# Performance work log

Measured on AMD Instinct MI355X. Metric: run time of the kernel, lower is better.

## Reference

```python
import jax, jax.numpy as jnp
import numpy as np
import math

# init kwargs (constants)
HSHIFT, VSHIFT, ANGLE = 2, 2, 2
BS, C, H, W = 2048, 1, 64, 64


def setup_inputs() -> dict:
    key = jax.random.key(0)
    k1, k2 = jax.random.split(key)
    fm1 = jax.random.normal(k1, (BS, C, H, W), dtype=jnp.float32)
    fm2 = jax.random.normal(k2, (BS, C, H, W), dtype=jnp.float32)
    return {"fm1": fm1, "fm2": fm2}


def _warp_rotate(img, theta_deg, h, w):
    """Equivalent of cv2.warpAffine(img, cv2.getRotationMatrix2D((w/2,h/2), theta, 1)).

    img: [bs, h, w]. Bilinear interpolation, constant-0 border.
    Returns (rotated_img [bs,h,w], rotated_ones_mask [h,w]).
    cv2 inverts the forward map internally; inverse of rotation by theta about
    the center is rotation by -theta about the center.
    """
    t = -theta_deg * (math.pi / 180.0)
    alpha = jnp.cos(t)
    beta = jnp.sin(t)
    cx, cy = w / 2.0, h / 2.0
    ys, xs = jnp.meshgrid(jnp.arange(h, dtype=jnp.float32),
                          jnp.arange(w, dtype=jnp.float32), indexing="ij")
    x_src = alpha * xs + beta * ys + (1.0 - alpha) * cx - beta * cy
    y_src = -beta * xs + alpha * ys + beta * cx + (1.0 - alpha) * cy

    x0 = jnp.floor(x_src)
    y0 = jnp.floor(y_src)
    wx = x_src - x0
    wy = y_src - y0
    x0i = x0.astype(jnp.int32)
    y0i = y0.astype(jnp.int32)

    out = jnp.zeros_like(img)
    msk = jnp.zeros((h, w), img.dtype)
    corners = ((0, 0, (1 - wy) * (1 - wx)), (0, 1, (1 - wy) * wx),
               (1, 0, wy * (1 - wx)), (1, 1, wy * wx))
    for dy, dx, wgt in corners:
        yi = y0i + dy
        xi = x0i + dx
        valid = ((yi >= 0) & (yi < h) & (xi >= 0) & (xi < w)).astype(img.dtype)
        yc = jnp.clip(yi, 0, h - 1)
        xc = jnp.clip(xi, 0, w - 1)
        out = out + (wgt * valid) * img[:, yc, xc]
        msk = msk + wgt * valid
    return out, msk


def _forward(fm1, fm2):
    bs, c, h, w = fm1.shape
    thetas = jnp.arange(-ANGLE, ANGLE + 1, dtype=jnp.float32)
    min_dist = jnp.full((bs,), jnp.finfo(jnp.float32).max, dtype=jnp.float32)
    for bh in range(-HSHIFT, HSHIFT + 1):
        for bv in range(-VSHIFT, VSHIFT + 1):
            if bh >= 0:
                r1, r2 = fm1[:, :, :, :w - bh], fm2[:, :, :, bh:]
            else:
                r1, r2 = fm1[:, :, :, -bh:], fm2[:, :, :, :w + bh]
            if bv >= 0:
                r1, r2 = r1[:, :, :h - bv, :], r2[:, :, bv:, :]
            else:
                r1, r2 = r1[:, :, -bv:, :], r2[:, :, :h + bv, :]
            oh, ow = r1.shape[2], r1.shape[3]
            r1s = r1[:, 0]  # [bs, oh, ow] (C==1)
            # original detaches ref2 before warping (cv2 path)
            r2s = jax.lax.stop_gradient(r2[:, 0])

            def one_theta(theta, r1s=r1s, r2s=r2s, oh=oh, ow=ow):
                rr2, mk = _warp_rotate(r2s, theta, oh, ow)
                se = ((r1s - rr2) ** 2) * mk  # [bs, oh, ow]
                return se.reshape(se.shape[0], -1).sum(1) / mk.sum()

            dists = jax.vmap(one_theta)(thetas)  # [ntheta, bs]
            min_dist = jnp.minimum(min_dist, dists.min(0))
    return min_dist


def reference(fm1, fm2):
    return _forward(fm1, fm2)
```

## Files before the change

kernel.cpp:

```cpp
#include <hip/hip_runtime.h>
#include <hip/hip_fp16.h>
#include <math.h>

#define NTH 5
#define GLO 66
#define GHI 132
#define PS (GLO + 4096 + GHI)

#define ALP0 0.99939082701909576f
#define ALP1 0.99984769515639127f
constexpr float ALPc[5] = {ALP0, ALP1, 1.0f, ALP1, ALP0};
constexpr float BETc[5] = {0.03489949670250097f, 0.01745240643728351f, 0.0f,
                           -0.01745240643728351f, -0.03489949670250097f};

__device__ __forceinline__ unsigned h2bits(float a, float b) {
    __half2 h = __floats2half2_rn(a, b);
    return *(unsigned*)&h;
}
__device__ __forceinline__ __half2 h2(unsigned u) { return *(__half2*)&u; }

__device__ __forceinline__ int pkadd(int a, int b) {
    __half2 r = __hadd2(*(__half2*)&a, *(__half2*)&b);
    return *(int*)&r;
}
__device__ __forceinline__ int hred16(__half2 v) {
    int x = *(int*)&v;
    int t = __builtin_amdgcn_update_dpp(0, x, 0xB1, 0xF, 0xF, true);
    x = pkadd(x, t);
    t = __builtin_amdgcn_update_dpp(0, x, 0x4E, 0xF, 0xF, true);
    x = pkadd(x, t);
    t = __builtin_amdgcn_update_dpp(0, x, 0x141, 0xF, 0xF, true);
    x = pkadd(x, t);
    t = __builtin_amdgcn_update_dpp(0, x, 0x140, 0xF, 0xF, true);
    x = pkadd(x, t);
    return x;
}

__global__ void pack_kernel(const float* __restrict__ fm1,
                            const float* __restrict__ fm2,
                            __half* __restrict__ fm1h,
                            __half* __restrict__ fm2h) {
    const int g = blockIdx.x;
    const int tid = threadIdx.x;
    const size_t inb = (size_t)g * 16 * 4096;
    for (int p = tid; p < 4096; p += 1024) {
        uint4 wa, wb, va, vb;
        wa.x = h2bits(fm1[inb + 0 * 4096 + p], fm1[inb + 1 * 4096 + p]);
        wa.y = h2bits(fm1[inb + 2 * 4096 + p], fm1[inb + 3 * 4096 + p]);
        wa.z = h2bits(fm1[inb + 4 * 4096 + p], fm1[inb + 5 * 4096 + p]);
        wa.w = h2bits(fm1[inb + 6 * 4096 + p], fm1[inb + 7 * 4096 + p]);
        wb.x = h2bits(fm1[inb + 8 * 4096 + p], fm1[inb + 9 * 4096 + p]);
        wb.y = h2bits(fm1[inb + 10 * 4096 + p], fm1[inb + 11 * 4096 + p]);
        wb.z = h2bits(fm1[inb + 12 * 4096 + p], fm1[inb + 13 * 4096 + p]);
        wb.w = h2bits(fm1[inb + 14 * 4096 + p], fm1[inb + 15 * 4096 + p]);
        va.x = h2bits(fm2[inb + 0 * 4096 + p], fm2[inb + 1 * 4096 + p]);
        va.y = h2bits(fm2[inb + 2 * 4096 + p], fm2[inb + 3 * 4096 + p]);
        va.z = h2bits(fm2[inb + 4 * 4096 + p], fm2[inb + 5 * 4096 + p]);
        va.w = h2bits(fm2[inb + 6 * 4096 + p], fm2[inb + 7 * 4096 + p]);
        vb.x = h2bits(fm2[inb + 8 * 4096 + p], fm2[inb + 9 * 4096 + p]);
        vb.y = h2bits(fm2[inb + 10 * 4096 + p], fm2[inb + 11 * 4096 + p]);
        vb.z = h2bits(fm2[inb + 12 * 4096 + p], fm2[inb + 13 * 4096 + p]);
        vb.w = h2bits(fm2[inb + 14 * 4096 + p], fm2[inb + 15 * 4096 + p]);
        *(uint4*)(fm1h + ((size_t)(g * 2 + 0) * 4096 + p) * 8) = wa;
        *(uint4*)(fm1h + ((size_t)(g * 2 + 1) * 4096 + p) * 8) = wb;
        *(uint4*)(fm2h + ((size_t)(g * 2 + 0) * 4096 + p) * 8) = va;
        *(uint4*)(fm2h + ((size_t)(g * 2 + 1) * 4096 + p) * 8) = vb;
    }
}

__global__ void table_kernel(uint4* __restrict__ tab, float* __restrict__ denom) {
    const int bid = blockIdx.x;
    const int s = bid >> 2, tj = bid & 3;
    const int ti = tj < 2 ? tj : tj + 1;
    const int tid = threadIdx.x;
    const int bh = (s / 5) - 2;
    const int bv = (s % 5) - 2;
    const int ox2 = bh >= 0 ? bh : 0;
    const int ow = 64 - (bh >= 0 ? bh : -bh);
    const int oy2 = bv >= 0 ? bv : 0;
    const int oh = 64 - (bv >= 0 ? bv : -bv);
    const float cx = 0.5f * (float)ow;
    const float cy = 0.5f * (float)oh;
    const float alpha = ALPc[ti], beta = BETc[ti];
    __shared__ float mred[4];
    float macc = 0.0f;
    for (int i = 0; i < 16; i++) {
        const int px = tid + 256 * i;
        const int y = px >> 6, x = px & 63;
        uint4 e = make_uint4(0u, 0u, 0u, (unsigned)GLO);
        if (x < ow && y < oh) {
            const float xs = (float)x, yf = (float)y;
            const float hx = fmaf(alpha, xs, (1.0f - alpha) * cx - beta * cy);
            const float hy = fmaf(-beta, xs, beta * cx + (1.0f - alpha) * cy);
            const float xsrc = fmaf(beta, yf, hx);
            const float ysrc = fmaf(alpha, yf, hy);
            const float x0f = floorf(xsrc), y0f = floorf(ysrc);
            const float wx = xsrc - x0f, wy = ysrc - y0f;
            const int x0 = (int)x0f, y0 = (int)y0f;
            const float ax0 = ((unsigned)x0 < (unsigned)ow) ? (1.f - wx) : 0.f;
            const float ax1 = ((unsigned)(x0 + 1) < (unsigned)ow) ? wx : 0.f;
            const float ay0 = ((unsigned)y0 < (unsigned)oh) ? (1.f - wy) : 0.f;
            const float ay1 = ((unsigned)(y0 + 1) < (unsigned)oh) ? wy : 0.f;
            const int x0c = min(max(x0, -1), ow - 1);
            const int y0c = min(max(y0, -1), oh - 1);
            const float mk = (ax0 + ax1) * (ay0 + ay1);
            e.x = h2bits(ay0 * ax0, ay0 * ax1);
            e.y = h2bits(ay1 * ax0, ay1 * ax1);
            e.z = h2bits(mk, 0.0f);
            e.w = (unsigned)(GLO + (y0c + oy2) * 64 + (x0c + ox2));
            macc += mk;
        }
        tab[(size_t)bid * 4096 + px] = e;
    }
    #pragma unroll
    for (int off = 32; off; off >>= 1) macc += __shfl_xor(macc, off);
    if ((tid & 63) == 0) mred[tid >> 6] = macc;
    __syncthreads();
    if (tid == 0) {
        denom[s * 5 + ti] = mred[0] + mred[1] + mred[2] + mred[3];
        if (tj == 0) denom[s * 5 + 2] = (float)(ow * oh);
    }
}

__launch_bounds__(1024, 8)
__global__ void wrsl_main(const __half* __restrict__ fm1h,
                          const __half* __restrict__ fm2h,
                          const uint4* __restrict__ tab,
                          const float* __restrict__ denom,
                          float* __restrict__ out) {
    __shared__ uint4 lds[PS];
    __shared__ float redm[16][4][40];
    __shared__ float colsum[40];

    const int tid = threadIdx.x;
    const int g = blockIdx.x >> 2;
    const int pl = (blockIdx.x >> 1) & 1;
    const int hf = blockIdx.x & 1;
    const int sBeg = hf ? 13 : 0;
    const int sEnd = hf ? 25 : 13;
    const size_t pbase = (size_t)(g * 2 + pl) * 4096;

    {
        const uint4* src = (const uint4*)(fm2h + pbase * 8);
        #pragma unroll
        for (int i = 0; i < 4; i++)
            lds[GLO + tid + 1024 * i] = src[tid + 1024 * i];
        if (tid < GLO + GHI) {
            const int off = (tid < GLO) ? tid : (4096 + tid);
            lds[off] = make_uint4(0u, 0u, 0u, 0u);
        }
    }
    const int lane = tid & 63, wid = tid >> 6;
    __syncthreads();

    float best = 3.4028234663852886e38f;

    for (int s = sBeg; s < sEnd; s++) {
        const int bh = (s / 5) - 2;
        const int bv = (s % 5) - 2;
        const int ox1 = bh >= 0 ? 0 : -bh;
        const int ox2 = bh >= 0 ? bh : 0;
        const int ow = 64 - (bh >= 0 ? bh : -bh);
        const int oy1 = bv >= 0 ? 0 : -bv;
        const int oy2 = bv >= 0 ? bv : 0;
        const int oh = 64 - (bv >= 0 ? bv : -bv);
        const int xcap = ox1 + min(lane, ow - 1);

        uint4 nr[4];
        #pragma unroll
        for (int k = 0; k < 4; k++) {
            const int p1 = (oy1 + min(wid + 16 * k, oh - 1)) * 64 + xcap;
            uint4 a = *(const uint4*)(fm1h + (pbase + p1) * 8);
            a.x ^= 0x80008000u; a.y ^= 0x80008000u; a.z ^= 0x80008000u; a.w ^= 0x80008000u;
            nr[k] = a;
        }

        const uint4* tqbase = tab + (size_t)(s * 4) * 4096;
        uint4 tv[4];
        #pragma unroll
        for (int k = 0; k < 4; k++)
            tv[k] = tqbase[(wid + 16 * k) * 64 + lane];

        {
            const float xinf = (lane < ow) ? 1.0f : 0.0f;
            const __half2 z2 = __float2half2_rn(0.0f);
            __half2 se[4] = {z2, z2, z2, z2};
            #pragma unroll
            for (int k = 0; k < 4; k++) {
                const int y = wid + 16 * k;
                const __half2 msk = __float2half2_rn((y < oh) ? xinf : 0.0f);
                const int idx = GLO + (oy2 + y) * 64 + ox2 + lane;
                const uint4 qa = lds[idx];
                #define LIGHT(SE, C)                                          \
                {                                                             \
                    __half2 d = __hmul2(__hadd2(h2(qa.C), h2(nr[k].C)), msk); \
                    SE = __hfma2(d, d, SE);                                   \
                }
                LIGHT(se[0], x) LIGHT(se[1], y) LIGHT(se[2], z) LIGHT(se[3], w)
                #undef LIGHT
            }
            int r0 = hred16(se[0]), r1 = hred16(se[1]);
            int r2 = hred16(se[2]), r3 = hred16(se[3]);
            if ((lane & 15) == 0) {
                float2 f0 = __half22float2(h2(r0)), f1 = __half22float2(h2(r1));
                float2 f2 = __half22float2(h2(r2)), f3 = __half22float2(h2(r3));
                float4* dst = (float4*)&redm[wid][lane >> 4][2 * 8];
                dst[0] = make_float4(f0.x, f0.y, f1.x, f1.y);
                dst[1] = make_float4(f2.x, f2.y, f3.x, f3.y);
            }
        }

        #pragma unroll
        for (int tj = 0; tj < 4; tj++) {
            const int ti = tj < 2 ? tj : tj + 1;
            uint4 tvn[4];
            if (tj < 3) {
                const uint4* tqn = tqbase + (size_t)(tj + 1) * 4096;
                #pragma unroll
                for (int k = 0; k < 4; k++)
                    tvn[k] = tqn[(wid + 16 * k) * 64 + lane];
            }

            const __half2 z2 = __float2half2_rn(0.0f);
            __half2 se[4] = {z2, z2, z2, z2};
            #pragma unroll
            for (int k = 0; k < 4; k++) {
                const __half2 tx = h2(tv[k].x), ty = h2(tv[k].y);
                const __half2 w00p = __low2half2(tx), w01p = __high2half2(tx);
                const __half2 w10p = __low2half2(ty), w11p = __high2half2(ty);
                const __half2 mkp = __low2half2(h2(tv[k].z));
                const int b0 = (int)tv[k].w;
                const uint4 q00 = lds[b0], q01 = lds[b0 + 1];
                const uint4 q10 = lds[b0 + 64], q11 = lds[b0 + 65];
                #define FULL(SE, C)                                        \
                {                                                          \
                    __half2 r = __hfma2(w00p, h2(q00.C), h2(nr[k].C));     \
                    r = __hfma2(w01p, h2(q01.C), r);                       \
                    r = __hfma2(w10p, h2(q10.C), r);                       \
                    r = __hfma2(w11p, h2(q11.C), r);                       \
                    SE = __hfma2(__hmul2(r, mkp), r, SE);                  \
                }
                FULL(se[0], x) FULL(se[1], y) FULL(se[2], z) FULL(se[3], w)
                #undef FULL
            }
            int r0 = hred16(se[0]), r1 = hred16(se[1]);
            int r2 = hred16(se[2]), r3 = hred16(se[3]);
            if ((lane & 15) == 0) {
                float2 f0 = __half22float2(h2(r0)), f1 = __half22float2(h2(r1));
                float2 f2 = __half22float2(h2(r2)), f3 = __half22float2(h2(r3));
                float4* dst = (float4*)&redm[wid][lane >> 4][ti * 8];
                dst[0] = make_float4(f0.x, f0.y, f1.x, f1.y);
                dst[1] = make_float4(f2.x, f2.y, f3.x, f3.y);
            }
            if (tj < 3) {
                #pragma unroll
                for (int k = 0; k < 4; k++) tv[k] = tvn[k];
            }
        }

        __syncthreads();
        if (tid < 40) {
            float sum = 0.0f;
            #pragma unroll 8
            for (int w = 0; w < 16; w++) {
                sum += redm[w][0][tid] + redm[w][1][tid] + redm[w][2][tid] + redm[w][3][tid];
            }
            colsum[tid] = sum;
        }
        __syncthreads();
        if (tid < 8) {
            #pragma unroll
            for (int t2 = 0; t2 < NTH; t2++)
                best = fminf(best, colsum[t2 * 8 + tid] / denom[s * 5 + t2]);
        }
    }
    if (tid < 8)
        atomicMin((unsigned int*)&out[g * 16 + pl * 8 + tid], __float_as_uint(best));
}

extern "C" void kernel_launch(void* const* d_in, const int* in_sizes, int n_in,
                              void* d_out, int out_size, void* d_ws, size_t ws_size,
                              hipStream_t stream) {
    const float* fm1 = (const float*)d_in[0];
    const float* fm2 = (const float*)d_in[1];
    float* out = (float*)d_out;
    __half* fm1h = (__half*)d_ws;
    __half* fm2h = (__half*)((char*)d_ws + (16u << 20));
    uint4* tab = (uint4*)((char*)d_ws + (32u << 20));
    float* denom = (float*)((char*)d_ws + (32u << 20) + 100u * 4096u * 16u);

    hipMemsetAsync(d_out, 0x7F, (size_t)out_size * 4, stream);
    pack_kernel<<<128, 1024, 0, stream>>>(fm1, fm2, fm1h, fm2h);
    table_kernel<<<100, 256, 0, stream>>>(tab, denom);
    wrsl_main<<<512, 1024, 0, stream>>>(fm1h, fm2h, tab, denom, out);
}
```

Measured before the change: 191.0 us.

## Split warp table into pre-broadcast weights and mask/index arrays, widen prep grids

Splits the per-pixel bilinear table into a 16-byte array of pre-broadcast half2 weights and an 8-byte mask/index array. This removes the per-use low/high broadcasts in the inner loop at the cost of more table bytes read per pixel. The pack and table kernels now launch twice and four times as many blocks, with denominators accumulated through atomicAdd after an extra memset. The main kernel's block index mapping is reordered so the same g is spread across distant blocks. The shift-only (light) path now reads fm2 from global memory instead of LDS.

```diff
diff --git a/kernel.cpp b/kernel.cpp
--- a/kernel.cpp
+++ b/kernel.cpp
@@ -40,10 +40,13 @@
                             const float* __restrict__ fm2,
                             __half* __restrict__ fm1h,
                             __half* __restrict__ fm2h) {
-    const int g = blockIdx.x;
+    const int g = blockIdx.x >> 1;
+    const int half = blockIdx.x & 1;
     const int tid = threadIdx.x;
     const size_t inb = (size_t)g * 16 * 4096;
-    for (int p = tid; p < 4096; p += 1024) {
+    #pragma unroll
+    for (int i = 0; i < 2; i++) {
+        const int p = half * 2048 + tid + 1024 * i;
         uint4 wa, wb, va, vb;
         wa.x = h2bits(fm1[inb + 0 * 4096 + p], fm1[inb + 1 * 4096 + p]);
         wa.y = h2bits(fm1[inb + 2 * 4096 + p], fm1[inb + 3 * 4096 + p]);
@@ -68,8 +71,10 @@
     }
 }
 
-__global__ void table_kernel(uint4* __restrict__ tab, float* __restrict__ denom) {
-    const int bid = blockIdx.x;
+__global__ void table_kernel(uint4* __restrict__ tabW, uint2* __restrict__ tabM,
+                             float* __restrict__ denom) {
+    const int bid = blockIdx.x >> 2;
+    const int quarter = blockIdx.x & 3;
     const int s = bid >> 2, tj = bid & 3;
     const int ti = tj < 2 ? tj : tj + 1;
     const int tid = threadIdx.x;
@@ -82,12 +87,12 @@
     const float cx = 0.5f * (float)ow;
     const float cy = 0.5f * (float)oh;
     const float alpha = ALPc[ti], beta = BETc[ti];
-    __shared__ float mred[4];
     float macc = 0.0f;
-    for (int i = 0; i < 16; i++) {
-        const int px = tid + 256 * i;
+    for (int i = 0; i < 4; i++) {
+        const int px = quarter * 1024 + tid + 256 * i;
         const int y = px >> 6, x = px & 63;
-        uint4 e = make_uint4(0u, 0u, 0u, (unsigned)GLO);
+        uint4 w = make_uint4(0u, 0u, 0u, 0u);
+        uint2 m = make_uint2(0u, (unsigned)GLO);
         if (x < ow && y < oh) {
             const float xs = (float)x, yf = (float)y;
             const float hx = fmaf(alpha, xs, (1.0f - alpha) * cx - beta * cy);
@@ -104,28 +109,34 @@
             const int x0c = min(max(x0, -1), ow - 1);
             const int y0c = min(max(y0, -1), oh - 1);
             const float mk = (ax0 + ax1) * (ay0 + ay1);
-            e.x = h2bits(ay0 * ax0, ay0 * ax1);
-            e.y = h2bits(ay1 * ax0, ay1 * ax1);
-            e.z = h2bits(mk, 0.0f);
-            e.w = (unsigned)(GLO + (y0c + oy2) * 64 + (x0c + ox2));
+            w.x = h2bits(ay0 * ax0, ay0 * ax0);
+            w.y = h2bits(ay0 * ax1, ay0 * ax1);
+            w.z = h2bits(ay1 * ax0, ay1 * ax0);
+            w.w = h2bits(ay1 * ax1, ay1 * ax1);
+            m.x = h2bits(mk, mk);
+            m.y = (unsigned)(GLO + (y0c + oy2) * 64 + (x0c + ox2));
             macc += mk;
         }
-        tab[(size_t)bid * 4096 + px] = e;
+        tabW[(size_t)bid * 4096 + px] = w;
+        tabM[(size_t)bid * 4096 + px] = m;
     }
     #pragma unroll
     for (int off = 32; off; off >>= 1) macc += __shfl_xor(macc, off);
+    __shared__ float mred[4];
     if ((tid & 63) == 0) mred[tid >> 6] = macc;
     __syncthreads();
     if (tid == 0) {
-        denom[s * 5 + ti] = mred[0] + mred[1] + mred[2] + mred[3];
-        if (tj == 0) denom[s * 5 + 2] = (float)(ow * oh);
+        atomicAdd(&denom[s * 5 + ti], mred[0] + mred[1] + mred[2] + mred[3]);
+        if (tj == 0 && quarter == 0)
+            denom[s * 5 + 2] = (float)(ow * oh);
     }
 }
 
 __launch_bounds__(1024, 8)
 __global__ void wrsl_main(const __half* __restrict__ fm1h,
                           const __half* __restrict__ fm2h,
-                          const uint4* __restrict__ tab,
+                          const uint4* __restrict__ tabW,
+                          const uint2* __restrict__ tabM,
                           const float* __restrict__ denom,
                           float* __restrict__ out) {
     __shared__ uint4 lds[PS];
@@ -133,9 +144,9 @@
     __shared__ float colsum[40];
 
     const int tid = threadIdx.x;
-    const int g = blockIdx.x >> 2;
-    const int pl = (blockIdx.x >> 1) & 1;
-    const int hf = blockIdx.x & 1;
+    const int g = blockIdx.x & 127;
+    const int pl = (blockIdx.x >> 7) & 1;
+    const int hf = (blockIdx.x >> 8) & 1;
     const int sBeg = hf ? 13 : 0;
     const int sEnd = hf ? 25 : 13;
     const size_t pbase = (size_t)(g * 2 + pl) * 4096;
@@ -175,11 +186,16 @@
             nr[k] = a;
         }
 
-        const uint4* tqbase = tab + (size_t)(s * 4) * 4096;
-        uint4 tv[4];
+        const uint4* twbase = tabW + (size_t)(s * 4) * 4096;
+        const uint2* tmbase = tabM + (size_t)(s * 4) * 4096;
+        uint4 tw[4];
+        uint2 tm[4];
         #pragma unroll
-        for (int k = 0; k < 4; k++)
-            tv[k] = tqbase[(wid + 16 * k) * 64 + lane];
+        for (int k = 0; k < 4; k++) {
+            const int e = (wid + 16 * k) * 64 + lane;
+            tw[k] = twbase[e];
+            tm[k] = tmbase[e];
+        }
 
         {
             const float xinf = (lane < ow) ? 1.0f : 0.0f;
@@ -189,8 +205,8 @@
             for (int k = 0; k < 4; k++) {
                 const int y = wid + 16 * k;
                 const __half2 msk = __float2half2_rn((y < oh) ? xinf : 0.0f);
-                const int idx = GLO + (oy2 + y) * 64 + ox2 + lane;
-                const uint4 qa = lds[idx];
+                const int idxp = (oy2 + min(y, oh - 1)) * 64 + ox2 + lane;
+                const uint4 qa = *(const uint4*)(fm2h + (pbase + idxp) * 8);
                 #define LIGHT(SE, C)                                          \
                 {                                                             \
                     __half2 d = __hmul2(__hadd2(h2(qa.C), h2(nr[k].C)), msk); \
@@ -213,23 +229,27 @@
         #pragma unroll
         for (int tj = 0; tj < 4; tj++) {
             const int ti = tj < 2 ? tj : tj + 1;
-            uint4 tvn[4];
+            uint4 twn[4];
+            uint2 tmn[4];
             if (tj < 3) {
-                const uint4* tqn = tqbase + (size_t)(tj + 1) * 4096;
+                const uint4* twq = twbase + (size_t)(tj + 1) * 4096;
+                const uint2* tmq = tmbase + (size_t)(tj + 1) * 4096;
                 #pragma unroll
-                for (int k = 0; k < 4; k++)
-                    tvn[k] = tqn[(wid + 16 * k) * 64 + lane];
+                for (int k = 0; k < 4; k++) {
+                    const int e = (wid + 16 * k) * 64 + lane;
+                    twn[k] = twq[e];
+                    tmn[k] = tmq[e];
+                }
             }
 
             const __half2 z2 = __float2half2_rn(0.0f);
             __half2 se[4] = {z2, z2, z2, z2};
             #pragma unroll
             for (int k = 0; k < 4; k++) {
-                const __half2 tx = h2(tv[k].x), ty = h2(tv[k].y);
-                const __half2 w00p = __low2half2(tx), w01p = __high2half2(tx);
-                const __half2 w10p = __low2half2(ty), w11p = __high2half2(ty);
-                const __half2 mkp = __low2half2(h2(tv[k].z));
-                const int b0 = (int)tv[k].w;
+                const __half2 w00p = h2(tw[k].x), w01p = h2(tw[k].y);
+                const __half2 w10p = h2(tw[k].z), w11p = h2(tw[k].w);
+                const __half2 mkp = h2(tm[k].x);
+                const int b0 = (int)tm[k].y;
                 const uint4 q00 = lds[b0], q01 = lds[b0 + 1];
                 const uint4 q10 = lds[b0 + 64], q11 = lds[b0 + 65];
                 #define FULL(SE, C)                                        \
@@ -254,7 +274,10 @@
             }
             if (tj < 3) {
                 #pragma unroll
-                for (int k = 0; k < 4; k++) tv[k] = tvn[k];
+                for (int k = 0; k < 4; k++) {
+                    tw[k] = twn[k];
+                    tm[k] = tmn[k];
+                }
             }
         }
 
@@ -284,13 +307,18 @@
     const float* fm1 = (const float*)d_in[0];
     const float* fm2 = (const float*)d_in[1];
     float* out = (float*)d_out;
+    const size_t TABW_OFF = (size_t)32 << 20;
+    const size_t TABM_OFF = TABW_OFF + (size_t)100 * 4096 * 16;
+    const size_t DEN_OFF = TABM_OFF + (size_t)100 * 4096 * 8;
     __half* fm1h = (__half*)d_ws;
-    __half* fm2h = (__half*)((char*)d_ws + (16u << 20));
-    uint4* tab = (uint4*)((char*)d_ws + (32u << 20));
-    float* denom = (float*)((char*)d_ws + (32u << 20) + 100u * 4096u * 16u);
+    __half* fm2h = (__half*)((char*)d_ws + ((size_t)16 << 20));
+    uint4* tabW = (uint4*)((char*)d_ws + TABW_OFF);
+    uint2* tabM = (uint2*)((char*)d_ws + TABM_OFF);
+    float* denom = (float*)((char*)d_ws + DEN_OFF);
 
     hipMemsetAsync(d_out, 0x7F, (size_t)out_size * 4, stream);
-    pack_kernel<<<128, 1024, 0, stream>>>(fm1, fm2, fm1h, fm2h);
-    table_kernel<<<100, 256, 0, stream>>>(tab, denom);
-    wrsl_main<<<512, 1024, 0, stream>>>(fm1h, fm2h, tab, denom, out);
-}
+    hipMemsetAsync(denom, 0, 125 * 4, stream);
+    pack_kernel<<<256, 1024, 0, stream>>>(fm1, fm2, fm1h, fm2h);
+    table_kernel<<<400, 256, 0, stream>>>(tabW, tabM, denom);
+    wrsl_main<<<512, 1024, 0, stream>>>(fm1h, fm2h, tabW, tabM, denom, out);
+}
```

After: 270.4 us. +41.6%, slower.
